# Performance work log

Hardware: AMD Instinct MI355X
Metric: run time of the kernel (lower is better)

## Reference

```python
import jax, jax.numpy as jnp
import numpy as np

B, S, D, H = 2, 2048, 1024, 16
DEPTH = D // H


def setup_inputs() -> dict:
    key = jax.random.key(0)
    ks = jax.random.split(key, 6)
    q = jax.random.normal(ks[0], (B, S, D), dtype=jnp.float32)
    k = jax.random.normal(ks[1], (B, S, D), dtype=jnp.float32)
    v = jax.random.normal(ks[2], (B, S, D), dtype=jnp.float32)
    # causal mask, broadcastable to [B, H, S, S]
    mask = jnp.tril(jnp.ones((S, S), dtype=bool))[None, None, :, :]
    wq = jax.random.normal(ks[3], (D, D), dtype=jnp.float32)
    wk = jax.random.normal(ks[4], (D, D), dtype=jnp.float32)
    wv = jax.random.normal(ks[5], (D, D), dtype=jnp.float32)
    return {"q": q, "k": k, "v": v, "mask": mask, "wq": wq, "wk": wk, "wv": wv}


def _split_heads(x):
    # [B, S, D] -> [B, H, S, depth]
    return x.reshape(x.shape[0], -1, H, DEPTH).transpose(0, 2, 1, 3)


def reference(q, k, v, mask, wq, wk, wv):
    q = _split_heads(q @ wq)
    k = _split_heads(k @ wk)
    v = _split_heads(v @ wv)
    scale = jnp.sqrt(jnp.float32(DEPTH))
    # [B, H, S, S]
    scores = jnp.einsum("bhqd,bhkd->bhqk", q, k) / scale
    scores = jnp.where(mask, scores, jnp.float32(-8.0))
    scores = scores - jnp.max(scores, axis=-1, keepdims=True)
    attn = jax.nn.softmax(scores, axis=-1)
    out = jnp.einsum("bhqk,bhkd->bhqd", attn, v)
    # [B, H, S, depth] -> [B, S, D]
    return out.transpose(0, 2, 1, 3).reshape(out.shape[0], -1, D)
```

## Files before the change

kernel.cpp:

```cpp
#include <hip/hip_runtime.h>
#include <hip/hip_bf16.h>

#define B_  2
#define S_  2048
#define D_  1024
#define H_  16
#define DH_ 64

typedef __attribute__((ext_vector_type(8)))  short  short8;
typedef __attribute__((ext_vector_type(4)))  short  short4b;
typedef __attribute__((ext_vector_type(16))) float  f32x16;

#define MFMA32(A,B,C) __builtin_amdgcn_mfma_f32_32x32x16_bf16(A,B,C,0,0,0)

static __device__ __forceinline__ short bf16b(float x) {
    __hip_bfloat16 h = __float2bfloat16(x);
    return *(short*)&h;
}
static __device__ __forceinline__ float bf16tof(short s) {
    union { unsigned u; float f; } cv;
    cv.u = ((unsigned)(unsigned short)s) << 16;
    return cv.f;
}
static __device__ __forceinline__ void gl2lds(const short* g, short* l) {
    __builtin_amdgcn_global_load_lds(
        (const __attribute__((address_space(1))) unsigned int*)g,
        (__attribute__((address_space(3))) unsigned int*)l, 16, 0, 0);
}

__global__ __launch_bounds__(256)
void conv_x(const float* __restrict__ q, const float* __restrict__ k,
            const float* __restrict__ v, char* __restrict__ ws) {
    const int z = blockIdx.y;
    const float* src = z == 0 ? q : z == 1 ? k : v;
    short* hi = (short*)(ws + (size_t)z * 16777216);
    short* lo = hi + 4194304;
    const int i = (blockIdx.x * 256 + threadIdx.x) * 4;
    float4 xv = *(const float4*)&src[i];
    const float* xf = (const float*)&xv;
    short4b h4, l4;
#pragma unroll
    for (int e = 0; e < 4; ++e) {
        short hb = bf16b(xf[e]);
        h4[e] = hb;
        l4[e] = bf16b(xf[e] - bf16tof(hb));
    }
    *(short4b*)&hi[i] = h4;
    *(short4b*)&lo[i] = l4;
}

__global__ __launch_bounds__(256)
void conv_wT(const float* __restrict__ wq, const float* __restrict__ wk,
             const float* __restrict__ wv, char* __restrict__ ws) {
    __shared__ short HiT[64][80];
    __shared__ short LoT[64][80];
    const int z = blockIdx.z;
    const float* w = z == 0 ? wq : z == 1 ? wk : wv;
    short* oh = (short*)(ws + 50331648 + (size_t)z * 4194304);
    short* ol = oh + 1048576;
    const int t  = threadIdx.x;
    const int k0 = blockIdx.x * 64, n0 = blockIdx.y * 64;

    const int kr = t >> 2, c4 = (t & 3) * 16;
    const float* srow = w + (size_t)(k0 + kr) * 1024 + n0 + c4;
#pragma unroll
    for (int u = 0; u < 16; u += 4) {
        float4 f = *(const float4*)&srow[u];
        const float* ff = (const float*)&f;
#pragma unroll
        for (int e = 0; e < 4; ++e) {
            int nl = c4 + u + e;
            short hb = bf16b(ff[e]);
            HiT[nl][kr] = hb;
            LoT[nl][kr] = bf16b(ff[e] - bf16tof(hb));
        }
    }
    __syncthreads();
    const int nl = t >> 2, kc = (t & 3) * 16;
    size_t off = (size_t)(n0 + nl) * 1024 + k0 + kc;
    *(short8*)&oh[off]     = *(const short8*)&HiT[nl][kc];
    *(short8*)&oh[off + 8] = *(const short8*)&HiT[nl][kc + 8];
    *(short8*)&ol[off]     = *(const short8*)&LoT[nl][kc];
    *(short8*)&ol[off + 8] = *(const short8*)&LoT[nl][kc + 8];
}

#define AHI_ 0
#define ALO_ 4096
#define BHI_ 8192
#define BLO_ 12288

__global__ __launch_bounds__(256, 2)
void proj_mfma(const short* __restrict__ xh0, const short* __restrict__ xl0,
               const short* __restrict__ xh1, const short* __restrict__ xl1,
               const short* __restrict__ xh2, const short* __restrict__ xl2,
               const short* __restrict__ wh0, const short* __restrict__ wl0,
               const short* __restrict__ wh1, const short* __restrict__ wl1,
               const short* __restrict__ wh2, const short* __restrict__ wl2,
               short* __restrict__ qh, short* __restrict__ ql,
               short* __restrict__ kh, short* __restrict__ kl,
               short* __restrict__ vt) {
    __shared__ __align__(16) short lds[32768];
    const int z  = blockIdx.z;
    const int m0 = blockIdx.y * 128;
    const int n0 = blockIdx.x * 128;
    const int t = threadIdx.x, lane = t & 63, w = t >> 6;
    const int l31 = lane & 31, hh = lane >> 5;

    const short* xh = z == 0 ? xh0 : z == 1 ? xh1 : xh2;
    const short* xl = z == 0 ? xl0 : z == 1 ? xl1 : xl2;
    const short* wh = z == 0 ? wh0 : z == 1 ? wh1 : wh2;
    const short* wl = z == 0 ? wl0 : z == 1 ? wl1 : wl2;

    const short* gsrc[8];
    short*       ldst[8];
#pragma unroll
    for (int j = 0; j < 8; ++j) {
        int sub = ((j & 1) << 2) | w;
        int cc  = (sub << 6) | lane;
        int row = cc >> 2, p = cc & 3;
        int kc  = p ^ ((row & 3) ^ ((row >> 2) & 3));
        bool isA  = j < 4;
        bool isHi = (j & 2) == 0;
        const short* base = isA ? (isHi ? xh : xl) : (isHi ? wh : wl);
        int r0g = isA ? m0 : n0;
        gsrc[j] = base + (size_t)(r0g + row) * 1024 + kc * 8;
        ldst[j] = &lds[(j >> 1) * 4096 + sub * 512];
    }

    const int rm0 = ((w & 1) << 6) + l31, rm1 = rm0 + 32;
    const int rn0 = ((w >> 1) << 6) + l31, rn1 = rn0 + 32;
    const int swm = (rm0 & 3) ^ ((rm0 >> 2) & 3);
    const int swn = (rn0 & 3) ^ ((rn0 >> 2) & 3);

    f32x16 accs[2][2] = {};

#pragma unroll
    for (int j = 0; j < 8; ++j)
        gl2lds(gsrc[j], ldst[j]);

    for (int kt = 0; kt < 32; ++kt) {
        const int cb = (kt & 1) << 14;
        if (kt < 31) {
            const int nb = 16384 - cb;
#pragma unroll
            for (int j = 0; j < 8; ++j)
                gl2lds(gsrc[j] + (kt + 1) * 32, ldst[j] + nb);
            asm volatile("s_waitcnt vmcnt(8)" ::: "memory");
        } else {
            asm volatile("s_waitcnt vmcnt(0)" ::: "memory");
        }
        __builtin_amdgcn_s_barrier();
        __builtin_amdgcn_sched_barrier(0);
        __builtin_amdgcn_s_setprio(1);
#pragma unroll
        for (int ks = 0; ks < 2; ++ks) {
            const int kc = (ks << 1) | hh;
            const int om = ((kc ^ swm) << 3) + cb;
            const int on = ((kc ^ swn) << 3) + cb;
            short8 ah0 = *(const short8*)&lds[AHI_ + rm0 * 32 + om];
            short8 ah1 = *(const short8*)&lds[AHI_ + rm1 * 32 + om];
            short8 al0 = *(const short8*)&lds[ALO_ + rm0 * 32 + om];
            short8 al1 = *(const short8*)&lds[ALO_ + rm1 * 32 + om];
            short8 bh0 = *(const short8*)&lds[BHI_ + rn0 * 32 + on];
            short8 bh1 = *(const short8*)&lds[BHI_ + rn1 * 32 + on];
            short8 bl0 = *(const short8*)&lds[BLO_ + rn0 * 32 + on];
            short8 bl1 = *(const short8*)&lds[BLO_ + rn1 * 32 + on];
            accs[0][0] = MFMA32(ah0, bh0, accs[0][0]);
            accs[0][1] = MFMA32(ah0, bh1, accs[0][1]);
            accs[1][0] = MFMA32(ah1, bh0, accs[1][0]);
            accs[1][1] = MFMA32(ah1, bh1, accs[1][1]);
            accs[0][0] = MFMA32(ah0, bl0, accs[0][0]);
            accs[0][1] = MFMA32(ah0, bl1, accs[0][1]);
            accs[1][0] = MFMA32(ah1, bl0, accs[1][0]);
            accs[1][1] = MFMA32(ah1, bl1, accs[1][1]);
            accs[0][0] = MFMA32(al0, bh0, accs[0][0]);
            accs[0][1] = MFMA32(al0, bh1, accs[0][1]);
            accs[1][0] = MFMA32(al1, bh0, accs[1][0]);
            accs[1][1] = MFMA32(al1, bh1, accs[1][1]);
        }
        __builtin_amdgcn_s_setprio(0);
        __builtin_amdgcn_sched_barrier(0);
        __builtin_amdgcn_s_barrier();
    }

    const int qm = w & 1, qn = w >> 1;
    const int bb = m0 >> 11;
    const int sbase = (m0 & 2047) + qm * 64;
    if (z < 2) {
        short* oh = z == 0 ? qh : kh;
        short* ol = z == 0 ? ql : kl;
#pragma unroll
        for (int mt = 0; mt < 2; ++mt)
#pragma unroll
        for (int nt = 0; nt < 2; ++nt) {
            int n_g = n0 + qn * 64 + nt * 32 + l31;
            int h = n_g >> 6, d = n_g & 63;
#pragma unroll
            for (int r = 0; r < 16; ++r) {
                int s = sbase + mt * 32 + (r & 3) + 8 * (r >> 2) + 4 * hh;
                size_t off = (((size_t)(bb * 16 + h) * 2048 + s) << 6) + d;
                float a = accs[mt][nt][r];
                short hb = bf16b(a);
                oh[off] = hb;
                ol[off] = bf16b(a - bf16tof(hb));
            }
        }
    } else {
#pragma unroll
        for (int mt = 0; mt < 2; ++mt)
#pragma unroll
        for (int nt = 0; nt < 2; ++nt) {
            int n_g = n0 + qn * 64 + nt * 32 + l31;
            int h = n_g >> 6, d = n_g & 63;
            size_t vbase = ((size_t)(bb * 16 + h) * 64 + d) * 2048;
#pragma unroll
            for (int r2 = 0; r2 < 4; ++r2) {
                int s0 = sbase + mt * 32 + 8 * r2 + 4 * hh;
                short4b pk;
#pragma unroll
                for (int a2 = 0; a2 < 4; ++a2)
                    pk[a2] = bf16b(accs[mt][nt][r2 * 4 + a2]);
                *(short4b*)&vt[vbase + s0] = pk;
            }
        }
    }
}

__global__ void vtile_sums(const short* __restrict__ Vt, float* __restrict__ TS) {
    int c = blockIdx.x, bh = blockIdx.y, d = threadIdx.x;
    const short* row = Vt + ((size_t)bh * DH_ + d) * S_ + c * 64;
    float s = 0.f;
    for (int j = 0; j < 64; ++j) s += bf16tof(row[j]);
    TS[((size_t)bh * 32 + c) * 64 + d] = s;
}

__global__ void suffix_scan(const float* __restrict__ TS, float* __restrict__ SV) {
    int bh = blockIdx.x, d = threadIdx.x;
    float run = 0.f;
    for (int c = 32; c >= 0; --c) {
        SV[((size_t)bh * 33 + c) * 64 + d] = run;
        if (c > 0) run += TS[((size_t)bh * 32 + (c - 1)) * 64 + d];
    }
}

__global__ __launch_bounds__(256, 2)
void attn_mfma(const short* __restrict__ Qhi, const short* __restrict__ Qlo,
               const short* __restrict__ Khi, const short* __restrict__ Klo,
               const short* __restrict__ Vt,  const float* __restrict__ SV,
               float* __restrict__ out) {
    __shared__ __align__(16) short KhiS[64 * 72];
    __shared__ __align__(16) short KloS[64 * 72];
    __shared__ __align__(16) short VtS [64 * 72];
    __shared__ __align__(16) short PS  [4][32 * 72];

    const int t     = threadIdx.x;
    const int lane  = t & 63;
    const int w     = t >> 6;
    const int l31   = lane & 31;
    const int hh    = lane >> 5;
    const int bh    = blockIdx.x;
    const int yy    = blockIdx.y;
    const int qt    = (yy < 8) ? yy : 23 - yy;
    const int q0    = qt * 128;
    const int myq   = q0 + w * 32 + l31;
    const int ktend = 2 * qt + 2;

    const size_t basebh = (size_t)bh * S_ * DH_;

    short8 qh[4], ql[4];
    {
        const short* qr = Qhi + basebh + (size_t)myq * DH_;
        const short* lr = Qlo + basebh + (size_t)myq * DH_;
#pragma unroll
        for (int kf = 0; kf < 4; ++kf) {
            int dofs = kf * 16 + hh * 8;
            qh[kf] = *(const short8*)(qr + dofs);
            ql[kf] = *(const short8*)(lr + dofs);
        }
    }

    float m_run = -INFINITY, l_run = 0.f;
    f32x16 oT0 = {}, oT1 = {};

    const int srow = t >> 2;
    const int sc16 = (t & 3) * 16;

    for (int kt = 0; kt < ktend; ++kt) {
        __syncthreads();
        {
            const short* gH = Khi + basebh + (size_t)(kt * 64 + srow) * 64 + sc16;
            const short* gL = Klo + basebh + (size_t)(kt * 64 + srow) * 64 + sc16;
            const short* gV = Vt + (size_t)bh * DH_ * S_ + (size_t)srow * S_ + kt * 64 + sc16;
            short8 a0 = *(const short8*)gH, a1 = *(const short8*)(gH + 8);
            short8 b0 = *(const short8*)gL, b1 = *(const short8*)(gL + 8);
            short8 c0 = *(const short8*)gV, c1 = *(const short8*)(gV + 8);
            *(short8*)&KhiS[srow * 72 + sc16]     = a0;
            *(short8*)&KhiS[srow * 72 + sc16 + 8] = a1;
            *(short8*)&KloS[srow * 72 + sc16]     = b0;
            *(short8*)&KloS[srow * 72 + sc16 + 8] = b1;
            *(short8*)&VtS [srow * 72 + sc16]     = c0;
            *(short8*)&VtS [srow * 72 + sc16 + 8] = c1;
        }
        __syncthreads();

        f32x16 acc0 = {}, acc1 = {};
#pragma unroll
        for (int kf = 0; kf < 4; ++kf) {
            int dofs = kf * 16 + hh * 8;
            short8 k0h = *(const short8*)&KhiS[(l31)      * 72 + dofs];
            short8 k0l = *(const short8*)&KloS[(l31)      * 72 + dofs];
            short8 k1h = *(const short8*)&KhiS[(l31 + 32) * 72 + dofs];
            short8 k1l = *(const short8*)&KloS[(l31 + 32) * 72 + dofs];
            acc0 = MFMA32(k0h, qh[kf], acc0);
            acc0 = MFMA32(k0h, ql[kf], acc0);
            acc0 = MFMA32(k0l, qh[kf], acc0);
            acc1 = MFMA32(k1h, qh[kf], acc1);
            acc1 = MFMA32(k1h, ql[kf], acc1);
            acc1 = MFMA32(k1l, qh[kf], acc1);
        }

        float vals[32];
        float tmax = -INFINITY;
#pragma unroll
        for (int r = 0; r < 16; ++r) {
            int key0 = kt * 64 + ((r & 3) + 8 * (r >> 2) + 4 * hh);
            float v0 = acc0[r] * 0.125f;
            v0 = (key0 <= myq) ? v0 : -8.0f;
            float v1 = acc1[r] * 0.125f;
            v1 = (key0 + 32 <= myq) ? v1 : -8.0f;
            vals[r] = v0;
            vals[16 + r] = v1;
            tmax = fmaxf(tmax, fmaxf(v0, v1));
        }
        tmax = fmaxf(tmax, __shfl_xor(tmax, 32, 64));
        float mnew  = fmaxf(m_run, tmax);
        float alpha = __expf(m_run - mnew);
        float psum  = 0.f;
#pragma unroll
        for (int mt = 0; mt < 2; ++mt)
#pragma unroll
            for (int b2 = 0; b2 < 4; ++b2) {
                short4b pk;
#pragma unroll
                for (int a = 0; a < 4; ++a) {
                    float p = __expf(vals[mt * 16 + b2 * 4 + a] - mnew);
                    short pb = bf16b(p);
                    psum += bf16tof(pb);
                    pk[a] = pb;
                }
                *(short4b*)&PS[w][l31 * 72 + mt * 32 + b2 * 8 + hh * 4] = pk;
            }
        psum += __shfl_xor(psum, 32, 64);
        l_run = l_run * alpha + psum;
        m_run = mnew;
#pragma unroll
        for (int r = 0; r < 16; ++r) { oT0[r] *= alpha; oT1[r] *= alpha; }

#pragma unroll
        for (int kf = 0; kf < 4; ++kf) {
            int kofs = kf * 16 + hh * 8;
            short8 pf = *(const short8*)&PS[w][l31 * 72 + kofs];
            short8 v0 = *(const short8*)&VtS[(l31)      * 72 + kofs];
            short8 v1 = *(const short8*)&VtS[(l31 + 32) * 72 + kofs];
            oT0 = MFMA32(v0, pf, oT0);
            oT1 = MFMA32(v1, pf, oT1);
        }
    }

    {
        float mfin = fmaxf(m_run, -8.0f);
        float aa   = __expf(m_run - mfin);
        float e8   = __expf(-8.0f - mfin);
        float nrem = (float)(S_ - ktend * 64);
        float lfin = l_run * aa + nrem * e8;
        float inv  = 1.0f / lfin;
        const float* sv = SV + ((size_t)bh * 33 + ktend) * 64;
#pragma unroll
        for (int r = 0; r < 16; ++r) {
            int dim0 = (r & 3) + 8 * (r >> 2) + 4 * hh;
            oT0[r] = (oT0[r] * aa + e8 * sv[dim0])      * inv;
            oT1[r] = (oT1[r] * aa + e8 * sv[dim0 + 32]) * inv;
        }
    }

    __syncthreads();
    float* Ob = (w == 0) ? (float*)KhiS :
                (w == 1) ? (float*)KloS :
                (w == 2) ? (float*)VtS  : (float*)PS;
#pragma unroll
    for (int r = 0; r < 16; ++r) {
        int dim0 = (r & 3) + 8 * (r >> 2) + 4 * hh;
        Ob[l31 * 68 + dim0]      = oT0[r];
        Ob[l31 * 68 + dim0 + 32] = oT1[r];
    }
    {
        const int qq = lane >> 1;
        const int ch = (lane & 1) * 32;
        const float* src = Ob + qq * 68 + ch;
        const int b  = bh >> 4;
        const int h  = bh & 15;
        float* dst = out + ((size_t)b * S_ + (q0 + w * 32 + qq)) * D_ + h * 64 + ch;
#pragma unroll
        for (int c = 0; c < 32; c += 4)
            *(float4*)(dst + c) = *(const float4*)(src + c);
    }
}

extern "C" void kernel_launch(void* const* d_in, const int* in_sizes, int n_in,
                              void* d_out, int out_size, void* d_ws, size_t ws_size,
                              hipStream_t stream) {
    const float* q  = (const float*)d_in[0];
    const float* k  = (const float*)d_in[1];
    const float* v  = (const float*)d_in[2];
    const float* wq = (const float*)d_in[4];
    const float* wk = (const float*)d_in[5];
    const float* wv = (const float*)d_in[6];
    float* out = (float*)d_out;

    char* ws = (char*)d_ws;
    const short* XH[3] = {(short*)ws, (short*)(ws + 16777216), (short*)(ws + 33554432)};
    const short* XL[3] = {XH[0] + 4194304, XH[1] + 4194304, XH[2] + 4194304};
    const short* WH[3] = {(short*)(ws + 50331648), (short*)(ws + 54525952), (short*)(ws + 58720256)};
    const short* WL[3] = {WH[0] + 1048576, WH[1] + 1048576, WH[2] + 1048576};
    float* TS = (float*)(ws + 62914560);
    float* SV = (float*)(ws + 62914560 + 262144);

    short* Qhi = (short*)d_in[0]; short* Qlo = Qhi + 4194304;
    short* Khi = (short*)d_in[1]; short* Klo = Khi + 4194304;
    short* Vt  = (short*)d_in[2];

    conv_x <<<dim3(4096, 3), 256, 0, stream>>>(q, k, v, ws);
    conv_wT<<<dim3(16, 16, 3), 256, 0, stream>>>(wq, wk, wv, ws);

    proj_mfma<<<dim3(8, 32, 3), 256, 0, stream>>>(
        XH[0], XL[0], XH[1], XL[1], XH[2], XL[2],
        WH[0], WL[0], WH[1], WL[1], WH[2], WL[2],
        Qhi, Qlo, Khi, Klo, Vt);

    vtile_sums<<<dim3(32, 32), 64, 0, stream>>>(Vt, TS);
    suffix_scan<<<32, 64, 0, stream>>>(TS, SV);

    attn_mfma<<<dim3(32, 16), 256, 0, stream>>>(Qhi, Qlo, Khi, Klo, Vt, SV, out);
}
```

Measured before the change: 286.9 us.

## Double-buffer K/V tiles via async global-to-LDS loads with swizzled layout and lazy rescale

The attention kernel now prefetches the next K/V tile straight into a second LDS buffer with gl2lds while the current tile is computed, waiting with explicit vmcnt counts. The padded row layout is replaced by an XOR-swizzled 64-wide layout so LDS reads stay bank-conflict-free. It also skips rescaling the output accumulators when the running max grows by no more than 8 (deferred max), sets wave priority around the MFMA blocks, and vectorises the V tile-sum kernel. The aim is to hide global load latency and trim softmax work, at the cost of twice the LDS and a correctness dependence on exact wait counts.

```diff
diff --git a/kernel.cpp b/kernel.cpp
--- a/kernel.cpp
+++ b/kernel.cpp
@@ -230,7 +230,12 @@
     int c = blockIdx.x, bh = blockIdx.y, d = threadIdx.x;
     const short* row = Vt + ((size_t)bh * DH_ + d) * S_ + c * 64;
     float s = 0.f;
-    for (int j = 0; j < 64; ++j) s += bf16tof(row[j]);
+#pragma unroll
+    for (int j = 0; j < 8; ++j) {
+        short8 v = *(const short8*)&row[j * 8];
+#pragma unroll
+        for (int e = 0; e < 8; ++e) s += bf16tof(v[e]);
+    }
     TS[((size_t)bh * 32 + c) * 64 + d] = s;
 }
 
@@ -248,9 +253,9 @@
                const short* __restrict__ Khi, const short* __restrict__ Klo,
                const short* __restrict__ Vt,  const float* __restrict__ SV,
                float* __restrict__ out) {
-    __shared__ __align__(16) short KhiS[64 * 72];
-    __shared__ __align__(16) short KloS[64 * 72];
-    __shared__ __align__(16) short VtS [64 * 72];
+    __shared__ __align__(16) short KhiS[8192];
+    __shared__ __align__(16) short KloS[8192];
+    __shared__ __align__(16) short VtS [8192];
     __shared__ __align__(16) short PS  [4][32 * 72];
 
     const int t     = threadIdx.x;
@@ -279,38 +284,55 @@
         }
     }
 
+    const int i1 = (w << 6) | lane;
+    const int i2 = 256 + i1;
+    const int r1 = i1 >> 3, c1 = (i1 & 7) ^ (r1 & 7);
+    const int r2 = i2 >> 3, c2 = (i2 & 7) ^ (r2 & 7);
+    const short* gKh1 = Khi + basebh + (size_t)r1 * 64 + c1 * 8;
+    const short* gKh2 = Khi + basebh + (size_t)r2 * 64 + c2 * 8;
+    const short* gKl1 = Klo + basebh + (size_t)r1 * 64 + c1 * 8;
+    const short* gKl2 = Klo + basebh + (size_t)r2 * 64 + c2 * 8;
+    const short* gV1  = Vt  + basebh + (size_t)r1 * S_ + c1 * 8;
+    const short* gV2  = Vt  + basebh + (size_t)r2 * S_ + c2 * 8;
+    const int wub = w << 9;
+
+#define ASTAGE(KT, BUF) do {                                                  \
+        const int ka_ = (KT) * 4096, va_ = (KT) * 64, bo_ = (BUF) * 4096;     \
+        gl2lds(gKh1 + ka_, &KhiS[bo_ + wub]);                                 \
+        gl2lds(gKh2 + ka_, &KhiS[bo_ + 2048 + wub]);                          \
+        gl2lds(gKl1 + ka_, &KloS[bo_ + wub]);                                 \
+        gl2lds(gKl2 + ka_, &KloS[bo_ + 2048 + wub]);                          \
+        gl2lds(gV1  + va_, &VtS [bo_ + wub]);                                 \
+        gl2lds(gV2  + va_, &VtS [bo_ + 2048 + wub]);                          \
+    } while (0)
+
     float m_run = -INFINITY, l_run = 0.f;
     f32x16 oT0 = {}, oT1 = {};
 
-    const int srow = t >> 2;
-    const int sc16 = (t & 3) * 16;
+    const int sw0 = l31 & 7;
+
+    ASTAGE(0, 0);
 
     for (int kt = 0; kt < ktend; ++kt) {
-        __syncthreads();
-        {
-            const short* gH = Khi + basebh + (size_t)(kt * 64 + srow) * 64 + sc16;
-            const short* gL = Klo + basebh + (size_t)(kt * 64 + srow) * 64 + sc16;
-            const short* gV = Vt + (size_t)bh * DH_ * S_ + (size_t)srow * S_ + kt * 64 + sc16;
-            short8 a0 = *(const short8*)gH, a1 = *(const short8*)(gH + 8);
-            short8 b0 = *(const short8*)gL, b1 = *(const short8*)(gL + 8);
-            short8 c0 = *(const short8*)gV, c1 = *(const short8*)(gV + 8);
-            *(short8*)&KhiS[srow * 72 + sc16]     = a0;
-            *(short8*)&KhiS[srow * 72 + sc16 + 8] = a1;
-            *(short8*)&KloS[srow * 72 + sc16]     = b0;
-            *(short8*)&KloS[srow * 72 + sc16 + 8] = b1;
-            *(short8*)&VtS [srow * 72 + sc16]     = c0;
-            *(short8*)&VtS [srow * 72 + sc16 + 8] = c1;
-        }
-        __syncthreads();
+        const int bo = (kt & 1) << 12;
+        if (kt + 1 < ktend) {
+            ASTAGE(kt + 1, (kt & 1) ^ 1);
+            asm volatile("s_waitcnt vmcnt(6)" ::: "memory");
+        } else {
+            asm volatile("s_waitcnt vmcnt(0)" ::: "memory");
+        }
+        __builtin_amdgcn_s_barrier();
+        __builtin_amdgcn_sched_barrier(0);
 
         f32x16 acc0 = {}, acc1 = {};
+        __builtin_amdgcn_s_setprio(1);
 #pragma unroll
         for (int kf = 0; kf < 4; ++kf) {
-            int dofs = kf * 16 + hh * 8;
-            short8 k0h = *(const short8*)&KhiS[(l31)      * 72 + dofs];
-            short8 k0l = *(const short8*)&KloS[(l31)      * 72 + dofs];
-            short8 k1h = *(const short8*)&KhiS[(l31 + 32) * 72 + dofs];
-            short8 k1l = *(const short8*)&KloS[(l31 + 32) * 72 + dofs];
+            const int cs = ((2 * kf + hh) ^ sw0) << 3;
+            short8 k0h = *(const short8*)&KhiS[bo + l31 * 64 + cs];
+            short8 k0l = *(const short8*)&KloS[bo + l31 * 64 + cs];
+            short8 k1h = *(const short8*)&KhiS[bo + (l31 + 32) * 64 + cs];
+            short8 k1l = *(const short8*)&KloS[bo + (l31 + 32) * 64 + cs];
             acc0 = MFMA32(k0h, qh[kf], acc0);
             acc0 = MFMA32(k0h, ql[kf], acc0);
             acc0 = MFMA32(k0l, qh[kf], acc0);
@@ -318,6 +340,7 @@
             acc1 = MFMA32(k1h, ql[kf], acc1);
             acc1 = MFMA32(k1l, qh[kf], acc1);
         }
+        __builtin_amdgcn_s_setprio(0);
 
         float vals[32];
         float tmax = -INFINITY;
@@ -333,9 +356,16 @@
             tmax = fmaxf(tmax, fmaxf(v0, v1));
         }
         tmax = fmaxf(tmax, __shfl_xor(tmax, 32, 64));
-        float mnew  = fmaxf(m_run, tmax);
-        float alpha = __expf(m_run - mnew);
-        float psum  = 0.f;
+        const bool defer = __all(tmax <= m_run + 8.0f);
+        if (!defer) {
+            float mnew  = fmaxf(m_run, tmax);
+            float alpha = __expf(m_run - mnew);
+            l_run *= alpha;
+#pragma unroll
+            for (int r = 0; r < 16; ++r) { oT0[r] *= alpha; oT1[r] *= alpha; }
+            m_run = mnew;
+        }
+        float psum = 0.f;
 #pragma unroll
         for (int mt = 0; mt < 2; ++mt)
 #pragma unroll
@@ -343,7 +373,7 @@
                 short4b pk;
 #pragma unroll
                 for (int a = 0; a < 4; ++a) {
-                    float p = __expf(vals[mt * 16 + b2 * 4 + a] - mnew);
+                    float p = __expf(vals[mt * 16 + b2 * 4 + a] - m_run);
                     short pb = bf16b(p);
                     psum += bf16tof(pb);
                     pk[a] = pb;
@@ -351,21 +381,24 @@
                 *(short4b*)&PS[w][l31 * 72 + mt * 32 + b2 * 8 + hh * 4] = pk;
             }
         psum += __shfl_xor(psum, 32, 64);
-        l_run = l_run * alpha + psum;
-        m_run = mnew;
-#pragma unroll
-        for (int r = 0; r < 16; ++r) { oT0[r] *= alpha; oT1[r] *= alpha; }
-
+        l_run += psum;
+
+        __builtin_amdgcn_s_setprio(1);
 #pragma unroll
         for (int kf = 0; kf < 4; ++kf) {
-            int kofs = kf * 16 + hh * 8;
+            const int kofs = kf * 16 + hh * 8;
+            const int cs = ((2 * kf + hh) ^ sw0) << 3;
             short8 pf = *(const short8*)&PS[w][l31 * 72 + kofs];
-            short8 v0 = *(const short8*)&VtS[(l31)      * 72 + kofs];
-            short8 v1 = *(const short8*)&VtS[(l31 + 32) * 72 + kofs];
+            short8 v0 = *(const short8*)&VtS[bo + l31 * 64 + cs];
+            short8 v1 = *(const short8*)&VtS[bo + (l31 + 32) * 64 + cs];
             oT0 = MFMA32(v0, pf, oT0);
             oT1 = MFMA32(v1, pf, oT1);
         }
-    }
+        __builtin_amdgcn_s_setprio(0);
+        __builtin_amdgcn_sched_barrier(0);
+        __builtin_amdgcn_s_barrier();
+    }
+#undef ASTAGE
 
     {
         float mfin = fmaxf(m_run, -8.0f);
```

Result: slower. 293.7 us (+2.4%).
